# Performance work log

Hardware: AMD Instinct MI355X
Metric: run time of the kernel (lower is better)

## Reference

```python
import jax, jax.numpy as jnp
import numpy as np
import math

H = 8                 # num_heads
MAX_REL = 32          # max_relative_distance
VOCAB_REL = 2 * MAX_REL + 1


def setup_inputs() -> dict:
    key = jax.random.key(0)
    ks = jax.random.split(key, 8)
    B, S, D = 4, 2048, 256
    hd = D // H
    sd = 1.0 / math.sqrt(D)
    inp = {
        "query": jax.random.normal(ks[0], (B, S, D), jnp.float32),
        "mask": jnp.ones((B, 1, 1, S), jnp.float32),
        "Wq": jax.random.normal(ks[1], (D, D), jnp.float32) * sd,
        "bq": jnp.zeros((D,), jnp.float32),
        "Wk": jax.random.normal(ks[2], (D, D), jnp.float32) * sd,
        "bk": jnp.zeros((D,), jnp.float32),
        "Wv": jax.random.normal(ks[3], (D, D), jnp.float32) * sd,
        "bv": jnp.zeros((D,), jnp.float32),
        "Wo": jax.random.normal(ks[4], (D, D), jnp.float32) * sd,
        "bo": jnp.zeros((D,), jnp.float32),
        "rel_table": jax.random.normal(ks[5], (VOCAB_REL, hd), jnp.float32) * 0.1,
    }
    return inp


def _split_heads(x, B, S, hd):
    # [B,S,D] -> [B,H,S,hd]
    return x.reshape(B, S, H, hd).transpose(0, 2, 1, 3)


def _relative_row_sums(S, rel_table):
    # Original: emb = table[relpos]  (S,S,hd); scores += einsum('bhid,jkd->bhijk', Q, emb).sum(-1)
    # == einsum('bhid,jd->bhij', Q, R) with R[j,d] = sum_k emb[j,k,d].
    # Compute R without materializing the (S,S,hd) tensor: count how often each
    # relative-position bucket appears in each row, then counts @ table.
    pos = jnp.arange(S)
    relpos = jnp.clip(pos[:, None] - pos[None, :], -MAX_REL, MAX_REL) + MAX_REL  # [S,S] ints
    rows = jnp.broadcast_to(pos[:, None], (S, S))
    counts = jnp.zeros((S, VOCAB_REL), rel_table.dtype).at[
        rows.reshape(-1), relpos.reshape(-1)
    ].add(1.0)
    return counts @ rel_table  # [S, hd]


def reference(query, mask, Wq, bq, Wk, bk, Wv, bv, Wo, bo, rel_table):
    B, S, D = query.shape
    hd = D // H
    scale = 1.0 / math.sqrt(hd)

    Q = _split_heads(query @ Wq + bq, B, S, hd)
    K = _split_heads(query @ Wk + bk, B, S, hd)   # key defaults to query
    V = _split_heads(query @ Wv + bv, B, S, hd)   # value defaults to key

    scores = jnp.einsum("bhid,bhjd->bhij", Q, K) * scale
    R = _relative_row_sums(S, rel_table)          # [S, hd]
    scores = scores + jnp.einsum("bhid,jd->bhij", Q, R)

    scores = scores + (1.0 - mask) * -1e9         # mask broadcast [B,1,1,S]
    attn = jax.nn.softmax(scores, axis=-1)        # dropout is identity (training=False)

    out = jnp.einsum("bhij,bhjd->bhid", attn, V)
    out = out.transpose(0, 2, 1, 3).reshape(B, S, D)
    return out @ Wo + bo
```

## Files before the change

### kernel.cpp

```cpp
#include <hip/hip_runtime.h>
#include <hip/hip_bf16.h>
#include <math.h>

#define NH 8
#define HD 32
#define SEQ 2048
#define DM 256
#define SCALE 0.17677669529663687f
#define INV_SCALE 5.656854249492381f
#define LOG2E 1.4426950408889634f
#define QSC (SCALE * LOG2E)
#define MNEG (-1e9f * LOG2E)

typedef float f32x4 __attribute__((ext_vector_type(4)));
typedef __bf16 bf16x8 __attribute__((ext_vector_type(8)));

#define GLOAD(g, l) __builtin_amdgcn_global_load_lds( \
    (const __attribute__((address_space(1))) void*)(g), \
    (__attribute__((address_space(3))) void*)(l), 16, 0, 0)

__global__ void k_prep(const float* __restrict__ mask,
                       const float* __restrict__ Wq, const float* __restrict__ Wk,
                       const float* __restrict__ Wv, const float* __restrict__ Wo,
                       const float* __restrict__ bq, const float* __restrict__ tbl,
                       __bf16* __restrict__ Wt, __bf16* __restrict__ WoT,
                       float* __restrict__ MT,
                       __bf16* __restrict__ SUFn, __bf16* __restrict__ PREn,
                       float* __restrict__ WV2T, float* __restrict__ cb,
                       int* __restrict__ MFLAG) {
  const int blk = blockIdx.x, tid = threadIdx.x;
  __shared__ float ts[64][65];
  __shared__ int okl;
  if (blk < 64) {
    const int idx = blk;
    const float* W;
    __bf16* dst;
    int tile;
    if (idx < 48) {
      int which = idx >> 4;
      W = which == 0 ? Wq : (which == 1 ? Wk : Wv);
      dst = Wt + which * 65536;
      tile = idx & 15;
    } else {
      W = Wo; dst = WoT; tile = idx - 48;
    }
    const int tr = (tile >> 2) * 64, tc = (tile & 3) * 64;
#pragma unroll
    for (int p = 0; p < 4; ++p) {
      int row = p * 16 + (tid >> 4);
      int col = (tid & 15) * 4;
      float4 v = *(const float4*)(W + (size_t)(tr + row) * 256 + tc + col);
      ts[row][col] = v.x; ts[row][col + 1] = v.y;
      ts[row][col + 2] = v.z; ts[row][col + 3] = v.w;
    }
    __syncthreads();
#pragma unroll
    for (int p = 0; p < 2; ++p) {
      int n = p * 32 + (tid >> 3);
      int kb = (tid & 7) * 8;
      union { __bf16 h[8]; bf16x8 v; } o;
#pragma unroll
      for (int e = 0; e < 8; ++e) o.h[e] = (__bf16)ts[kb + e][n];
      *(bf16x8*)(dst + (size_t)(tc + n) * 256 + tr + kb) = o.v;
    }
  } else if (blk == 64) {
    if (tid == 0) okl = 1;
    __syncthreads();
    bool ok = true;
    for (int i = tid; i < 4 * SEQ; i += 256) {
      float mv = mask[i];
      MT[i] = (1.0f - mv) * MNEG;
      ok &= (mv == 1.0f);
    }
    if (!ok) atomicAnd(&okl, 0);
    __syncthreads();
    if (tid == 0) MFLAG[0] = okl;
  } else if (blk == 65) {
    for (int idx = tid; idx < 1024; idx += 256) {
      int j = idx >> 5, d = idx & 31;
      float s = 0.f;
      for (int u = j + 33; u <= 63; ++u) s += tbl[u * 32 + d];
      SUFn[idx] = (__bf16)(-s * INV_SCALE);
    }
    for (int idx = tid; idx < 1024; idx += 256) {
      int jj = idx >> 5, d = idx & 31;
      float s = 0.f;
      for (int u = 1; u <= jj; ++u) s += tbl[u * 32 + d];
      PREn[idx] = (__bf16)(-s * INV_SCALE);
    }
  } else if (blk < 82) {
    int tg = (blk - 66) * 256 + tid;
    int hv = tg >> 8, k = tg & 255;
    const float* T = tbl + ((hv & 1) ? 0 : 64 * 32);
    const float* w = Wq + (size_t)k * 256 + (hv >> 1) * 32;
    float acc = 0.f;
#pragma unroll
    for (int d = 0; d < 32; ++d) acc = fmaf(w[d], T[d], acc);
    WV2T[hv * 256 + k] = acc * LOG2E;
  } else {
    if (tid < 16) {
      const float* T = tbl + ((tid & 1) ? 0 : 64 * 32);
      float a = 0.f;
#pragma unroll
      for (int d = 0; d < 32; ++d) a = fmaf(bq[(tid >> 1) * 32 + d], T[d], a);
      cb[tid] = a * LOG2E;
    }
  }
}

__launch_bounds__(256)
__global__ void k_rel(const float* __restrict__ X, const float* __restrict__ WV2T,
                      const float* __restrict__ cb, float* __restrict__ REL,
                      __bf16* __restrict__ Xb) {
  __shared__ float Xs[32][260];
  __shared__ float Ws[16][260];
  const int tid = threadIdx.x;
  const size_t base = (size_t)blockIdx.x * 32 * 256;
#pragma unroll
  for (int p = 0; p < 8; ++p) {
    int idx = p * 1024 + tid * 4;
    float4 v = *(const float4*)(X + base + idx);
    *(float4*)&Xs[idx >> 8][idx & 255] = v;
  }
#pragma unroll
  for (int p = 0; p < 4; ++p) {
    int idx = p * 1024 + tid * 4;
    float4 v = *(const float4*)(WV2T + idx);
    *(float4*)&Ws[idx >> 8][idx & 255] = v;
  }
  __syncthreads();
#pragma unroll
  for (int p = 0; p < 4; ++p) {
    int idx = p * 2048 + tid * 8;
    int row = idx >> 8, col = idx & 255;
    float4 a = *(const float4*)&Xs[row][col];
    float4 b4 = *(const float4*)&Xs[row][col + 4];
    union { __bf16 h[8]; bf16x8 v; } o;
    o.h[0] = (__bf16)a.x;  o.h[1] = (__bf16)a.y;
    o.h[2] = (__bf16)a.z;  o.h[3] = (__bf16)a.w;
    o.h[4] = (__bf16)b4.x; o.h[5] = (__bf16)b4.y;
    o.h[6] = (__bf16)b4.z; o.h[7] = (__bf16)b4.w;
    *(bf16x8*)(Xb + base + idx) = o.v;
  }
  const int hv = tid & 15, rl = tid >> 4;
  float a0 = cb[hv], a1 = a0;
  const float* xs0 = &Xs[rl][0];
  const float* xs1 = &Xs[rl + 16][0];
  const float* wsp = &Ws[hv][0];
#pragma unroll 8
  for (int k = 0; k < 256; ++k) {
    float w = wsp[k];
    a0 = fmaf(xs0[k], w, a0);
    a1 = fmaf(xs1[k], w, a1);
  }
  const int row0 = blockIdx.x * 32 + rl;
  const int h = hv >> 1, v = hv & 1;
  const int b0i = row0 >> 11, s0 = row0 & 2047;
  REL[((size_t)(b0i * NH + h) * SEQ + s0) * 2 + v] = a0;
  const int r1 = row0 + 16;
  const int b1i = r1 >> 11, s1 = r1 & 2047;
  REL[((size_t)(b1i * NH + h) * SEQ + s1) * 2 + v] = a1;
}

template <int MODE>
__launch_bounds__(256)
__global__ void k_gemm(const __bf16* __restrict__ A, const __bf16* __restrict__ Bt,
                       const float* __restrict__ b0, const float* __restrict__ b1,
                       const float* __restrict__ b2,
                       __bf16* __restrict__ Qb, __bf16* __restrict__ Kb,
                       __bf16* __restrict__ VTout, float* __restrict__ Y) {
  constexpr int BM = (MODE == 0) ? 128 : 64;
  constexpr int FI = BM / 32;
  __shared__ __align__(16) __bf16 As[BM * 64];
  __shared__ __align__(16) __bf16 Bs[64 * 64];
  const int tid = threadIdx.x, lane = tid & 63, wid = tid >> 6;
  const int l16 = lane & 15, lhi = lane >> 4;
  const int wr = wid >> 1, wc = wid & 1;
  const int m0 = blockIdx.x * BM, n0 = blockIdx.y * 64;

  f32x4 acc[FI][2];
#pragma unroll
  for (int i = 0; i < FI; ++i)
#pragma unroll
    for (int j = 0; j < 2; ++j) acc[i][j] = (f32x4){0.f, 0.f, 0.f, 0.f};

  for (int k0 = 0; k0 < 256; k0 += 64) {
    __syncthreads();
#pragma unroll
    for (int cc = 0; cc < BM / 32; ++cc) {
      int cl = tid + cc * 256;
      int row = cl >> 3, kc = cl & 7;
      int k = k0 + ((kc ^ (row & 7)) * 8);
      const __bf16* src;
      if constexpr (MODE == 0) {
        src = A + (size_t)(m0 + row) * 256 + k;
      } else {
        int r = m0 + row, bb = r >> 11, s = r & 2047, h = k >> 5, dh = k & 31;
        src = A + ((size_t)(bb * NH + h) * SEQ + s) * HD + dh;
      }
      GLOAD(src, (__bf16*)As + (size_t)cl * 8);
    }
#pragma unroll
    for (int cc = 0; cc < 2; ++cc) {
      int cl = tid + cc * 256;
      int row = cl >> 3, kc = cl & 7;
      int k = k0 + ((kc ^ (row & 7)) * 8);
      GLOAD(Bt + (size_t)(n0 + row) * 256 + k, (__bf16*)Bs + (size_t)cl * 8);
    }
    __syncthreads();
#pragma unroll
    for (int kk = 0; kk < 64; kk += 32) {
      bf16x8 af[FI], bfr[2];
#pragma unroll
      for (int fi = 0; fi < FI; ++fi) {
        int row = wr * (BM / 2) + fi * 16 + l16;
        af[fi] = *(const bf16x8*)(As + row * 64 + ((((kk >> 3) + lhi) ^ (row & 7)) * 8));
      }
#pragma unroll
      for (int fj = 0; fj < 2; ++fj) {
        int row = wc * 32 + fj * 16 + l16;
        bfr[fj] = *(const bf16x8*)(Bs + row * 64 + ((((kk >> 3) + lhi) ^ (row & 7)) * 8));
      }
#pragma unroll
      for (int fi = 0; fi < FI; ++fi)
#pragma unroll
        for (int fj = 0; fj < 2; ++fj)
          acc[fi][fj] = __builtin_amdgcn_mfma_f32_16x16x32_bf16(af[fi], bfr[fj], acc[fi][fj], 0, 0, 0);
    }
  }
#pragma unroll
  for (int fi = 0; fi < FI; ++fi) {
#pragma unroll
    for (int fj = 0; fj < 2; ++fj) {
      int mrow = m0 + wr * (BM / 2) + fi * 16 + lhi * 4;
      int ncol = n0 + wc * 32 + fj * 16 + l16;
      if constexpr (MODE == 0) {
        int which = ncol >> 8, nw = ncol & 255, h = nw >> 5, dh = nw & 31;
        int bb = mrow >> 11, s0 = mrow & 2047;
        if (which == 2) {
          union { __bf16 h4[4]; uint2 u; } o;
#pragma unroll
          for (int r = 0; r < 4; ++r) o.h4[r] = (__bf16)(acc[fi][fj][r] + b2[nw]);
          *(uint2*)(VTout + ((size_t)(bb * NH + h) * HD + dh) * SEQ + s0) = o.u;
        } else {
          const float* bias = which == 0 ? b0 : b1;
#pragma unroll
          for (int r = 0; r < 4; ++r) {
            float v = acc[fi][fj][r] + bias[nw];
            size_t oi = ((size_t)(bb * NH + h) * SEQ + (s0 + r)) * HD + dh;
            if (which == 0) Qb[oi] = (__bf16)(v * QSC);
            else Kb[oi] = (__bf16)v;
          }
        }
      } else {
#pragma unroll
        for (int r = 0; r < 4; ++r)
          Y[(size_t)(mrow + r) * 256 + ncol] = acc[fi][fj][r] + b0[ncol];
      }
    }
  }
}

__launch_bounds__(512, 4)
__global__ void k_flash(const __bf16* __restrict__ Qb, const __bf16* __restrict__ Kb,
                        const __bf16* __restrict__ VT, const float* __restrict__ REL,
                        const __bf16* __restrict__ SUFn, const __bf16* __restrict__ PREn,
                        const float* __restrict__ MT, const int* __restrict__ MFLAG,
                        __bf16* __restrict__ Ob) {
  const int bid = blockIdx.x;
  const int bh = (bid & 7) * 4 + ((bid >> 3) & 3);
  const int qt = bid >> 5;
  const int b = bh >> 3;
  const int tid = threadIdx.x, wid = tid >> 6, lane = tid & 63;
  const int l16 = lane & 15, lhi = lane >> 4;

  __shared__ __align__(16) __bf16 kbuf[2][256 * 32];
  __shared__ __align__(16) __bf16 vbuf[2][32 * 256];
  __shared__ __align__(16) __bf16 plds[8][16 * 64];

  const int qrow = qt * 128 + wid * 16 + l16;
  const size_t rg = (size_t)bh * SEQ + qrow;
  const bf16x8 qfrag = *(const bf16x8*)(Qb + rg * HD + lhi * 8);
  const float2 uw = *(const float2*)(REL + rg * 2);
  const float uu = uw.x, ww = uw.y, duw = uu - ww;
  const float duw16 = 16.f * duw;
  const f32x4 duwr = {0.f, duw, 2.f * duw, 3.f * duw};
  const int flag = MFLAG[0];

  const int u0 = tid, u1 = tid + 512;
  const int kj0 = u0 >> 2, kc0 = u0 & 3, kj1 = u1 >> 2, kc1 = u1 & 3;
  const __bf16* ksrc0 = Kb + ((size_t)bh * SEQ + kj0) * HD + ((kc0 ^ ((kj0 >> 1) & 3)) * 8);
  const __bf16* ksrc1 = Kb + ((size_t)bh * SEQ + kj1) * HD + ((kc1 ^ ((kj1 >> 1) & 3)) * 8);
  const int vd0 = u0 >> 5, vc0 = u0 & 31, vd1 = u1 >> 5, vc1 = u1 & 31;
  const __bf16* vsrc0 = VT + ((size_t)bh * HD + vd0) * SEQ + ((vc0 ^ (vd0 & 7)) * 8);
  const __bf16* vsrc1 = VT + ((size_t)bh * HD + vd1) * SEQ + ((vc1 ^ (vd1 & 7)) * 8);

  f32x4 of0 = {0.f, 0.f, 0.f, 0.f}, of1 = {0.f, 0.f, 0.f, 0.f}, of2 = {0.f, 0.f, 0.f, 0.f};
  bf16x8 ones;
#pragma unroll
  for (int e = 0; e < 8; ++e) ones[e] = (__bf16)1.0f;
  float m = -3.0e38f;
  __bf16* pl = &plds[wid][0];
  const float* mtp = MT + b * SEQ + lhi * 4;

  GLOAD(ksrc0, &kbuf[0][(size_t)u0 * 8]);
  GLOAD(ksrc1, &kbuf[0][(size_t)u1 * 8]);
  GLOAD(vsrc0, &vbuf[0][(size_t)u0 * 8]);
  GLOAD(vsrc1, &vbuf[0][(size_t)u1 * 8]);
  __syncthreads();

  for (int mt = 0, cur = 0; mt < 8; ++mt, cur ^= 1) {
    if (mt < 7) {
      const int nb = cur ^ 1;
      GLOAD(ksrc0 + (size_t)(mt + 1) * 8192, &kbuf[nb][(size_t)u0 * 8]);
      GLOAD(ksrc1 + (size_t)(mt + 1) * 8192, &kbuf[nb][(size_t)u1 * 8]);
      GLOAD(vsrc0 + (mt + 1) * 256, &vbuf[nb][(size_t)u0 * 8]);
      GLOAD(vsrc1 + (mt + 1) * 256, &vbuf[nb][(size_t)u1 * 8]);
    }
    const __bf16* kb = kbuf[cur];
    const __bf16* vb = vbuf[cur];

#pragma unroll
    for (int sub = 0; sub < 2; ++sub) {
      const int jb = mt * 256 + sub * 128;

      f32x4 lin = duwr + (float)(jb + lhi * 4) * duw;
      f32x4 sf[8];
      __builtin_amdgcn_s_setprio(1);
#pragma unroll
      for (int jt = 0; jt < 8; ++jt) {
        const int row = sub * 128 + jt * 16 + l16;
        bf16x8 kf = *(const bf16x8*)(kb + row * 32 + ((lhi ^ ((row >> 1) & 3)) * 8));
        sf[jt] = __builtin_amdgcn_mfma_f32_16x16x32_bf16(kf, qfrag, lin, 0, 0, 0);
        lin += duw16;
      }
      __builtin_amdgcn_s_setprio(0);

      if (jb == 0) {
        const bf16x8 s0 = *(const bf16x8*)(SUFn + l16 * HD + lhi * 8);
        const bf16x8 s1 = *(const bf16x8*)(SUFn + (16 + l16) * HD + lhi * 8);
        sf[0] = __builtin_amdgcn_mfma_f32_16x16x32_bf16(s0, qfrag, sf[0], 0, 0, 0);
        sf[1] = __builtin_amdgcn_mfma_f32_16x16x32_bf16(s1, qfrag, sf[1], 0, 0, 0);
#pragma unroll
        for (int jt = 0; jt < 2; ++jt)
#pragma unroll
          for (int r = 0; r < 4; ++r)
            sf[jt][r] += fmaxf(31.f - (float)(jt * 16 + lhi * 4 + r), 0.f) * uu;
      }
      if (jb == SEQ - 128) {
        const bf16x8 p0 = *(const bf16x8*)(PREn + l16 * HD + lhi * 8);
        const bf16x8 p1 = *(const bf16x8*)(PREn + (16 + l16) * HD + lhi * 8);
        sf[6] = __builtin_amdgcn_mfma_f32_16x16x32_bf16(p0, qfrag, sf[6], 0, 0, 0);
        sf[7] = __builtin_amdgcn_mfma_f32_16x16x32_bf16(p1, qfrag, sf[7], 0, 0, 0);
#pragma unroll
        for (int jt = 6; jt < 8; ++jt)
#pragma unroll
          for (int r = 0; r < 4; ++r)
            sf[jt][r] += fmaxf((float)(jb + jt * 16 + lhi * 4 + r) - 2016.f, 0.f) * ww;
      }
      if (!flag) {
#pragma unroll
        for (int jt = 0; jt < 8; ++jt)
          sf[jt] += *(const f32x4*)(mtp + jb + jt * 16);
      }

      float tmax = -3.0e38f;
#pragma unroll
      for (int jt = 0; jt < 8; ++jt)
        tmax = fmaxf(tmax, fmaxf(fmaxf(sf[jt].x, sf[jt].y), fmaxf(sf[jt].z, sf[jt].w)));
      tmax = fmaxf(tmax, __shfl_xor(tmax, 16));
      tmax = fmaxf(tmax, __shfl_xor(tmax, 32));
      const float mn = fmaxf(m, tmax);
      const float c = __builtin_amdgcn_exp2f(m - mn);
      m = mn;
      of0 *= c; of1 *= c; of2 *= c;

#pragma unroll
      for (int ph = 0; ph < 2; ++ph) {
#pragma unroll
        for (int jt = ph * 4; jt < ph * 4 + 4; ++jt) {
          union { __bf16 h4[4]; uint2 u; } pk;
#pragma unroll
          for (int r = 0; r < 4; ++r)
            pk.h4[r] = (__bf16)__builtin_amdgcn_exp2f(sf[jt][r] - m);
          const int blk16 = (((jt & 3) * 2 + (lhi >> 1)) ^ (l16 & 7));
          *(uint2*)(pl + l16 * 64 + blk16 * 8 + (lhi & 1) * 4) = pk.u;
        }
        __builtin_amdgcn_s_setprio(1);
#pragma unroll
        for (int kt = ph * 2; kt < ph * 2 + 2; ++kt) {
          const int pblk = (((kt & 1) * 4 + lhi) ^ (l16 & 7));
          bf16x8 pf = *(const bf16x8*)(pl + l16 * 64 + pblk * 8);
          const int G = sub * 16 + kt * 4 + lhi;
          bf16x8 v0 = *(const bf16x8*)(vb + l16 * 256 + ((G ^ (l16 & 7)) * 8));
          bf16x8 v1 = *(const bf16x8*)(vb + (16 + l16) * 256 + ((G ^ (l16 & 7)) * 8));
          of0 = __builtin_amdgcn_mfma_f32_16x16x32_bf16(v0, pf, of0, 0, 0, 0);
          of1 = __builtin_amdgcn_mfma_f32_16x16x32_bf16(v1, pf, of1, 0, 0, 0);
          of2 = __builtin_amdgcn_mfma_f32_16x16x32_bf16(ones, pf, of2, 0, 0, 0);
        }
        __builtin_amdgcn_s_setprio(0);
      }
    }
    __syncthreads();
  }

  const float inv = 1.0f / of2[0];
  union { __bf16 h4[4]; uint2 u; } o0, o1;
#pragma unroll
  for (int r = 0; r < 4; ++r) {
    o0.h4[r] = (__bf16)(of0[r] * inv);
    o1.h4[r] = (__bf16)(of1[r] * inv);
  }
  *(uint2*)(Ob + rg * HD + lhi * 4) = o0.u;
  *(uint2*)(Ob + rg * HD + 16 + lhi * 4) = o1.u;
}

extern "C" void kernel_launch(void* const* d_in, const int* in_sizes, int n_in,
                              void* d_out, int out_size, void* d_ws, size_t ws_size,
                              hipStream_t stream) {
  (void)in_sizes; (void)n_in; (void)out_size; (void)ws_size;
  const float* query = (const float*)d_in[0];
  const float* mask  = (const float*)d_in[1];
  const float* Wq = (const float*)d_in[2];
  const float* bq = (const float*)d_in[3];
  const float* Wk = (const float*)d_in[4];
  const float* bk = (const float*)d_in[5];
  const float* Wv = (const float*)d_in[6];
  const float* bv = (const float*)d_in[7];
  const float* Wo = (const float*)d_in[8];
  const float* bo = (const float*)d_in[9];
  const float* tbl = (const float*)d_in[10];
  float* out = (float*)d_out;
  char* ws = (char*)d_ws;

  const size_t MB = 1024ull * 1024;
  __bf16* Xb    = (__bf16*)(ws);
  __bf16* Wt    = (__bf16*)(ws + 4 * MB);
  __bf16* WoT   = (__bf16*)(ws + 4 * MB + 393216);
  __bf16* SUFn  = (__bf16*)(ws + 4 * MB + 524288);
  __bf16* PREn  = (__bf16*)(ws + 4 * MB + 526336);
  float*  WV2T  = (float*) (ws + 4 * MB + 528384);
  float*  cbv   = (float*) (ws + 4 * MB + 544768);
  float*  MT    = (float*) (ws + 4 * MB + 544832);
  int*    MFLAG = (int*)   (ws + 4 * MB + 577600);
  float*  REL   = (float*) (ws + 5 * MB);
  __bf16* Qb    = (__bf16*)(ws + 6 * MB);
  __bf16* Kb    = (__bf16*)(ws + 10 * MB);
  __bf16* VT    = (__bf16*)(ws + 14 * MB);
  __bf16* Ob    = (__bf16*)(ws + 18 * MB);

  k_prep<<<83, 256, 0, stream>>>(mask, Wq, Wk, Wv, Wo, bq, tbl,
                                 Wt, WoT, MT, SUFn, PREn, WV2T, cbv, MFLAG);
  k_rel<<<256, 256, 0, stream>>>(query, WV2T, cbv, REL, Xb);
  k_gemm<0><<<dim3(64, 12), 256, 0, stream>>>(Xb, Wt, bq, bk, bv, Qb, Kb, VT, nullptr);
  k_flash<<<512, 512, 0, stream>>>(Qb, Kb, VT, REL, SUFn, PREn, MT, MFLAG, Ob);
  k_gemm<1><<<dim3(128, 4), 256, 0, stream>>>(Ob, WoT, bo, nullptr, nullptr,
                                              nullptr, nullptr, nullptr, out);
}
```

Baseline: 92.27 us.

## Shrink flash KV tile to 128 keys and fold linear bias into precomputed offsets

The flash-attention kernel now stages 128-key K/V tiles instead of 256, which halves LDS use and uses one async load per thread per tile. The per-tile linear relative-position term is precomputed once as constant accumulator seeds. The tile-dependent offset is applied to the running max rather than being added to every score. This trims VALU work in the inner loop and frees LDS for occupancy, at the cost of twice as many barriers and prefetch rounds. Subtracting the shifted max keeps the math equivalent, but it may change rounding slightly.

New measurement: 91.64 us. Within noise of the previous version (-0.7%).

```diff
diff --git a/kernel.cpp b/kernel.cpp
--- a/kernel.cpp
+++ b/kernel.cpp
@@ -274,8 +274,8 @@
   const int tid = threadIdx.x, wid = tid >> 6, lane = tid & 63;
   const int l16 = lane & 15, lhi = lane >> 4;
 
-  __shared__ __align__(16) __bf16 kbuf[2][256 * 32];
-  __shared__ __align__(16) __bf16 vbuf[2][32 * 256];
+  __shared__ __align__(16) __bf16 kbuf[2][128 * 32];
+  __shared__ __align__(16) __bf16 vbuf[2][32 * 128];
   __shared__ __align__(16) __bf16 plds[8][16 * 64];
 
   const int qrow = qt * 128 + wid * 16 + l16;
@@ -283,17 +283,22 @@
   const bf16x8 qfrag = *(const bf16x8*)(Qb + rg * HD + lhi * 8);
   const float2 uw = *(const float2*)(REL + rg * 2);
   const float uu = uw.x, ww = uw.y, duw = uu - ww;
-  const float duw16 = 16.f * duw;
-  const f32x4 duwr = {0.f, duw, 2.f * duw, 3.f * duw};
+  const float duw128 = 128.f * duw;
   const int flag = MFLAG[0];
 
-  const int u0 = tid, u1 = tid + 512;
-  const int kj0 = u0 >> 2, kc0 = u0 & 3, kj1 = u1 >> 2, kc1 = u1 & 3;
-  const __bf16* ksrc0 = Kb + ((size_t)bh * SEQ + kj0) * HD + ((kc0 ^ ((kj0 >> 1) & 3)) * 8);
-  const __bf16* ksrc1 = Kb + ((size_t)bh * SEQ + kj1) * HD + ((kc1 ^ ((kj1 >> 1) & 3)) * 8);
-  const int vd0 = u0 >> 5, vc0 = u0 & 31, vd1 = u1 >> 5, vc1 = u1 & 31;
-  const __bf16* vsrc0 = VT + ((size_t)bh * HD + vd0) * SEQ + ((vc0 ^ (vd0 & 7)) * 8);
-  const __bf16* vsrc1 = VT + ((size_t)bh * HD + vd1) * SEQ + ((vc1 ^ (vd1 & 7)) * 8);
+  f32x4 c0[8];
+  {
+    const f32x4 cr = {(float)(lhi * 4) * duw, (float)(lhi * 4 + 1) * duw,
+                      (float)(lhi * 4 + 2) * duw, (float)(lhi * 4 + 3) * duw};
+#pragma unroll
+    for (int jt = 0; jt < 8; ++jt)
+      c0[jt] = cr + (float)(jt * 16) * duw;
+  }
+
+  const int kj = tid >> 2, kc = tid & 3;
+  const __bf16* ksrc = Kb + ((size_t)bh * SEQ + kj) * HD + ((kc ^ ((kj >> 1) & 3)) * 8);
+  const int vd = tid >> 4, vc = tid & 15;
+  const __bf16* vsrc = VT + ((size_t)bh * HD + vd) * SEQ + ((vc ^ (vd & 7)) * 8);
 
   f32x4 of0 = {0.f, 0.f, 0.f, 0.f}, of1 = {0.f, 0.f, 0.f, 0.f}, of2 = {0.f, 0.f, 0.f, 0.f};
   bf16x8 ones;
@@ -303,103 +308,93 @@
   __bf16* pl = &plds[wid][0];
   const float* mtp = MT + b * SEQ + lhi * 4;
 
-  GLOAD(ksrc0, &kbuf[0][(size_t)u0 * 8]);
-  GLOAD(ksrc1, &kbuf[0][(size_t)u1 * 8]);
-  GLOAD(vsrc0, &vbuf[0][(size_t)u0 * 8]);
-  GLOAD(vsrc1, &vbuf[0][(size_t)u1 * 8]);
+  GLOAD(ksrc, &kbuf[0][(size_t)tid * 8]);
+  GLOAD(vsrc, &vbuf[0][(size_t)tid * 8]);
   __syncthreads();
 
-  for (int mt = 0, cur = 0; mt < 8; ++mt, cur ^= 1) {
-    if (mt < 7) {
-      const int nb = cur ^ 1;
-      GLOAD(ksrc0 + (size_t)(mt + 1) * 8192, &kbuf[nb][(size_t)u0 * 8]);
-      GLOAD(ksrc1 + (size_t)(mt + 1) * 8192, &kbuf[nb][(size_t)u1 * 8]);
-      GLOAD(vsrc0 + (mt + 1) * 256, &vbuf[nb][(size_t)u0 * 8]);
-      GLOAD(vsrc1 + (mt + 1) * 256, &vbuf[nb][(size_t)u1 * 8]);
+  for (int t = 0, cur = 0; t < 16; ++t, cur ^= 1) {
+    const int jb = t * 128;
+    if (t < 15) {
+      GLOAD(ksrc + (size_t)(jb + 128) * HD, &kbuf[cur ^ 1][(size_t)tid * 8]);
+      GLOAD(vsrc + (jb + 128), &vbuf[cur ^ 1][(size_t)tid * 8]);
     }
     const __bf16* kb = kbuf[cur];
     const __bf16* vb = vbuf[cur];
 
-#pragma unroll
-    for (int sub = 0; sub < 2; ++sub) {
-      const int jb = mt * 256 + sub * 128;
-
-      f32x4 lin = duwr + (float)(jb + lhi * 4) * duw;
-      f32x4 sf[8];
+    f32x4 sf[8];
+    __builtin_amdgcn_s_setprio(1);
+#pragma unroll
+    for (int jt = 0; jt < 8; ++jt) {
+      const int row = jt * 16 + l16;
+      bf16x8 kf = *(const bf16x8*)(kb + row * 32 + ((lhi ^ ((row >> 1) & 3)) * 8));
+      sf[jt] = __builtin_amdgcn_mfma_f32_16x16x32_bf16(kf, qfrag, c0[jt], 0, 0, 0);
+    }
+    __builtin_amdgcn_s_setprio(0);
+
+    if (t == 0) {
+      const bf16x8 s0 = *(const bf16x8*)(SUFn + l16 * HD + lhi * 8);
+      const bf16x8 s1 = *(const bf16x8*)(SUFn + (16 + l16) * HD + lhi * 8);
+      sf[0] = __builtin_amdgcn_mfma_f32_16x16x32_bf16(s0, qfrag, sf[0], 0, 0, 0);
+      sf[1] = __builtin_amdgcn_mfma_f32_16x16x32_bf16(s1, qfrag, sf[1], 0, 0, 0);
+#pragma unroll
+      for (int jt = 0; jt < 2; ++jt)
+#pragma unroll
+        for (int r = 0; r < 4; ++r)
+          sf[jt][r] += fmaxf(31.f - (float)(jt * 16 + lhi * 4 + r), 0.f) * uu;
+    }
+    if (t == 15) {
+      const bf16x8 p0 = *(const bf16x8*)(PREn + l16 * HD + lhi * 8);
+      const bf16x8 p1 = *(const bf16x8*)(PREn + (16 + l16) * HD + lhi * 8);
+      sf[6] = __builtin_amdgcn_mfma_f32_16x16x32_bf16(p0, qfrag, sf[6], 0, 0, 0);
+      sf[7] = __builtin_amdgcn_mfma_f32_16x16x32_bf16(p1, qfrag, sf[7], 0, 0, 0);
+#pragma unroll
+      for (int jt = 6; jt < 8; ++jt)
+#pragma unroll
+        for (int r = 0; r < 4; ++r)
+          sf[jt][r] += fmaxf((float)(jb + jt * 16 + lhi * 4 + r) - 2016.f, 0.f) * ww;
+    }
+    if (!flag) {
+#pragma unroll
+      for (int jt = 0; jt < 8; ++jt)
+        sf[jt] += *(const f32x4*)(mtp + jb + jt * 16);
+    }
+
+    const float tsp = (float)jb * duw; (void)duw128;
+    float tmax = -3.0e38f;
+#pragma unroll
+    for (int jt = 0; jt < 8; ++jt)
+      tmax = fmaxf(fmaxf(fmaxf(fmaxf(tmax, sf[jt].x), sf[jt].y), sf[jt].z), sf[jt].w);
+    tmax = fmaxf(tmax, __shfl_xor(tmax, 16));
+    tmax = fmaxf(tmax, __shfl_xor(tmax, 32));
+    const float mn = fmaxf(m, tmax + tsp);
+    const float c = __builtin_amdgcn_exp2f(m - mn);
+    m = mn;
+    const float m2 = mn - tsp;
+    of0 *= c; of1 *= c; of2 *= c;
+
+#pragma unroll
+    for (int ph = 0; ph < 2; ++ph) {
+#pragma unroll
+      for (int jt = ph * 4; jt < ph * 4 + 4; ++jt) {
+        union { __bf16 h4[4]; uint2 u; } pk;
+#pragma unroll
+        for (int r = 0; r < 4; ++r)
+          pk.h4[r] = (__bf16)__builtin_amdgcn_exp2f(sf[jt][r] - m2);
+        const int blk16 = (((jt & 3) * 2 + (lhi >> 1)) ^ (l16 & 7));
+        *(uint2*)(pl + l16 * 64 + blk16 * 8 + (lhi & 1) * 4) = pk.u;
+      }
       __builtin_amdgcn_s_setprio(1);
 #pragma unroll
-      for (int jt = 0; jt < 8; ++jt) {
-        const int row = sub * 128 + jt * 16 + l16;
-        bf16x8 kf = *(const bf16x8*)(kb + row * 32 + ((lhi ^ ((row >> 1) & 3)) * 8));
-        sf[jt] = __builtin_amdgcn_mfma_f32_16x16x32_bf16(kf, qfrag, lin, 0, 0, 0);
-        lin += duw16;
+      for (int kt = ph * 2; kt < ph * 2 + 2; ++kt) {
+        const int pblk = (((kt & 1) * 4 + lhi) ^ (l16 & 7));
+        bf16x8 pf = *(const bf16x8*)(pl + l16 * 64 + pblk * 8);
+        bf16x8 v0 = *(const bf16x8*)(vb + l16 * 128 + (((kt * 4 + lhi) ^ (l16 & 7)) * 8));
+        bf16x8 v1 = *(const bf16x8*)(vb + (16 + l16) * 128 + (((kt * 4 + lhi) ^ (l16 & 7)) * 8));
+        of0 = __builtin_amdgcn_mfma_f32_16x16x32_bf16(v0, pf, of0, 0, 0, 0);
+        of1 = __builtin_amdgcn_mfma_f32_16x16x32_bf16(v1, pf, of1, 0, 0, 0);
+        of2 = __builtin_amdgcn_mfma_f32_16x16x32_bf16(ones, pf, of2, 0, 0, 0);
       }
       __builtin_amdgcn_s_setprio(0);
-
-      if (jb == 0) {
-        const bf16x8 s0 = *(const bf16x8*)(SUFn + l16 * HD + lhi * 8);
-        const bf16x8 s1 = *(const bf16x8*)(SUFn + (16 + l16) * HD + lhi * 8);
-        sf[0] = __builtin_amdgcn_mfma_f32_16x16x32_bf16(s0, qfrag, sf[0], 0, 0, 0);
-        sf[1] = __builtin_amdgcn_mfma_f32_16x16x32_bf16(s1, qfrag, sf[1], 0, 0, 0);
-#pragma unroll
-        for (int jt = 0; jt < 2; ++jt)
-#pragma unroll
-          for (int r = 0; r < 4; ++r)
-            sf[jt][r] += fmaxf(31.f - (float)(jt * 16 + lhi * 4 + r), 0.f) * uu;
-      }
-      if (jb == SEQ - 128) {
-        const bf16x8 p0 = *(const bf16x8*)(PREn + l16 * HD + lhi * 8);
-        const bf16x8 p1 = *(const bf16x8*)(PREn + (16 + l16) * HD + lhi * 8);
-        sf[6] = __builtin_amdgcn_mfma_f32_16x16x32_bf16(p0, qfrag, sf[6], 0, 0, 0);
-        sf[7] = __builtin_amdgcn_mfma_f32_16x16x32_bf16(p1, qfrag, sf[7], 0, 0, 0);
-#pragma unroll
-        for (int jt = 6; jt < 8; ++jt)
-#pragma unroll
-          for (int r = 0; r < 4; ++r)
-            sf[jt][r] += fmaxf((float)(jb + jt * 16 + lhi * 4 + r) - 2016.f, 0.f) * ww;
-      }
-      if (!flag) {
-#pragma unroll
-        for (int jt = 0; jt < 8; ++jt)
-          sf[jt] += *(const f32x4*)(mtp + jb + jt * 16);
-      }
-
-      float tmax = -3.0e38f;
-#pragma unroll
-      for (int jt = 0; jt < 8; ++jt)
-        tmax = fmaxf(tmax, fmaxf(fmaxf(sf[jt].x, sf[jt].y), fmaxf(sf[jt].z, sf[jt].w)));
-      tmax = fmaxf(tmax, __shfl_xor(tmax, 16));
-      tmax = fmaxf(tmax, __shfl_xor(tmax, 32));
-      const float mn = fmaxf(m, tmax);
-      const float c = __builtin_amdgcn_exp2f(m - mn);
-      m = mn;
-      of0 *= c; of1 *= c; of2 *= c;
-
-#pragma unroll
-      for (int ph = 0; ph < 2; ++ph) {
-#pragma unroll
-        for (int jt = ph * 4; jt < ph * 4 + 4; ++jt) {
-          union { __bf16 h4[4]; uint2 u; } pk;
-#pragma unroll
-          for (int r = 0; r < 4; ++r)
-            pk.h4[r] = (__bf16)__builtin_amdgcn_exp2f(sf[jt][r] - m);
-          const int blk16 = (((jt & 3) * 2 + (lhi >> 1)) ^ (l16 & 7));
-          *(uint2*)(pl + l16 * 64 + blk16 * 8 + (lhi & 1) * 4) = pk.u;
-        }
-        __builtin_amdgcn_s_setprio(1);
-#pragma unroll
-        for (int kt = ph * 2; kt < ph * 2 + 2; ++kt) {
-          const int pblk = (((kt & 1) * 4 + lhi) ^ (l16 & 7));
-          bf16x8 pf = *(const bf16x8*)(pl + l16 * 64 + pblk * 8);
-          const int G = sub * 16 + kt * 4 + lhi;
-          bf16x8 v0 = *(const bf16x8*)(vb + l16 * 256 + ((G ^ (l16 & 7)) * 8));
-          bf16x8 v1 = *(const bf16x8*)(vb + (16 + l16) * 256 + ((G ^ (l16 & 7)) * 8));
-          of0 = __builtin_amdgcn_mfma_f32_16x16x32_bf16(v0, pf, of0, 0, 0, 0);
-          of1 = __builtin_amdgcn_mfma_f32_16x16x32_bf16(v1, pf, of1, 0, 0, 0);
-          of2 = __builtin_amdgcn_mfma_f32_16x16x32_bf16(ones, pf, of2, 0, 0, 0);
-        }
-        __builtin_amdgcn_s_setprio(0);
-      }
     }
     __syncthreads();
   }
```
